# Performance work log

Hardware: AMD Instinct MI355X
Metric: run time of the kernel (lower is better)

Reference implementation:

```python
import jax, jax.numpy as jnp
import numpy as np

N = 100000
E = 1600000
NFEAT = 128
NHID = 128
NCLASS = 10


def setup_inputs() -> dict:
    key = jax.random.key(0)
    ks = jax.random.split(key, 12)
    x = jax.random.normal(ks[0], (N, NFEAT), dtype=jnp.float32)
    edge_index = jax.random.randint(ks[1], (2, E), 0, N, dtype=jnp.int64)
    s = 0.05
    W1 = jax.random.normal(ks[2], (NFEAT, NHID), dtype=jnp.float32) * s
    b1 = jnp.zeros((NHID,), dtype=jnp.float32)
    W2 = jax.random.normal(ks[3], (NHID, NHID), dtype=jnp.float32) * s
    b2 = jnp.zeros((NHID,), dtype=jnp.float32)
    W3 = jax.random.normal(ks[4], (NHID, NHID), dtype=jnp.float32) * s
    b3 = jnp.zeros((NHID,), dtype=jnp.float32)
    Wl = jax.random.normal(ks[5], (NHID, NCLASS), dtype=jnp.float32) * s
    bl = jnp.zeros((NCLASS,), dtype=jnp.float32)
    return {"x": x, "edge_index": edge_index, "W1": W1, "b1": b1,
            "W2": W2, "b2": b2, "W3": W3, "b3": b3, "Wl": Wl, "bl": bl}


def _gcn_norm(edge_index, num_nodes):
    # PyG gcn_norm with add_self_loops=True and unit edge weights.
    loops = jnp.arange(num_nodes, dtype=edge_index.dtype)
    src = jnp.concatenate([edge_index[0], loops])  # [E+N]
    dst = jnp.concatenate([edge_index[1], loops])
    ones = jnp.ones(src.shape[0], dtype=jnp.float32)
    deg = jax.ops.segment_sum(ones, dst, num_segments=num_nodes)
    dis = jax.lax.rsqrt(deg)  # deg >= 1 due to self-loops
    norm = dis[src] * dis[dst]  # [E+N]
    return src, dst, norm


def _gcn_conv(h, src, dst, norm, W, b, num_nodes):
    h = h @ W                                   # [N, out]
    msg = h[src] * norm[:, None]                # gather + edge scaling
    out = jax.ops.segment_sum(msg, dst, num_segments=num_nodes)
    return out + b


def reference(x, edge_index, W1, b1, W2, b2, W3, b3, Wl, bl):
    src, dst, norm = _gcn_norm(edge_index, N)
    h = jax.nn.relu(_gcn_conv(x, src, dst, norm, W1, b1, N))
    h = jax.nn.relu(_gcn_conv(h, src, dst, norm, W2, b2, N))
    h = _gcn_conv(h, src, dst, norm, W3, b3, N)
    logits = h @ Wl + bl                        # dropout is identity (eval / p=0)
    return jax.nn.log_softmax(logits, axis=1)
```

## Files before the change

### kernel.cpp

```cpp
#include <hip/hip_runtime.h>

#define NFEAT 128
#define NCLS  10
#define NCP   16
#define BROW  512
#define BINC  4096

static inline size_t alignup(size_t x) { return (x + 255) & ~size_t(255); }

__device__ __forceinline__ ushort f2bf(float f) {
  uint x = __float_as_uint(f);
  return (ushort)((x + 0x7fffu + ((x >> 16) & 1u)) >> 16);
}
__device__ __forceinline__ float bf2f(ushort u) {
  return __uint_as_float(((uint)u) << 16);
}

typedef short bf16x8 __attribute__((ext_vector_type(8)));
typedef float f32x4 __attribute__((ext_vector_type(4)));


__global__ void zero_ints(int* __restrict__ p, int n) {
  int i = blockIdx.x * 256 + threadIdx.x;
  if (i < n) p[i] = 0;
}

__global__ __launch_bounds__(256) void bucket_hist(const int* __restrict__ dst,
                                                   int* __restrict__ bkt_cnt,
                                                   int e, int nbkt) {
  __shared__ int hist[256];
  for (int t = threadIdx.x; t < nbkt; t += 256) hist[t] = 0;
  __syncthreads();
  int i = blockIdx.x * 256 + threadIdx.x;
  int stride = gridDim.x * 256;
  for (; i < e; i += stride) atomicAdd(&hist[dst[i] >> 9], 1);
  __syncthreads();
  for (int t = threadIdx.x; t < nbkt; t += 256)
    if (hist[t]) atomicAdd(&bkt_cnt[t], hist[t]);
}

__global__ __launch_bounds__(256) void bkt_scan(const int* __restrict__ bkt_cnt,
                                                int* __restrict__ bkt_off,
                                                int* __restrict__ gfrontier,
                                                int n, int nbkt) {
  __shared__ int sbuf[256];
  const int t = threadIdx.x;
  int x = 0;
  if (t < nbkt) {
    int lo = t << 9;
    int nodes = n - lo; if (nodes > BROW) nodes = BROW;
    x = bkt_cnt[t] + nodes;
  }
  sbuf[t] = x;
  __syncthreads();
  for (int off = 1; off < 256; off <<= 1) {
    int v = (t >= off) ? sbuf[t - off] : 0;
    __syncthreads();
    sbuf[t] += v;
    __syncthreads();
  }
  if (t < nbkt) { bkt_off[t] = sbuf[t] - x; gfrontier[t] = sbuf[t] - x; }
  if (t == nbkt - 1) bkt_off[nbkt] = sbuf[t];
}

__global__ __launch_bounds__(256) void bin_items(const int* __restrict__ ei,
                                                 int nE, int total, int nbkt,
                                                 int* __restrict__ gfrontier,
                                                 int2* __restrict__ binned) {
  __shared__ int hist[256];
  __shared__ int loff[256];
  __shared__ int gbase[256];
  __shared__ int sbuf[256];
  __shared__ int2 st[BINC];
  const int t = threadIdx.x;
  const int chunk0 = blockIdx.x * BINC;
  for (int q = t; q < nbkt; q += 256) hist[q] = 0;
  __syncthreads();
  for (int j = t; j < BINC; j += 256) {
    int i = chunk0 + j;
    if (i < total) {
      int d = (i < nE) ? ei[nE + i] : (i - nE);
      atomicAdd(&hist[d >> 9], 1);
    }
  }
  __syncthreads();
  int x = (t < nbkt) ? hist[t] : 0;
  sbuf[t] = x;
  __syncthreads();
  for (int off = 1; off < 256; off <<= 1) {
    int v = (t >= off) ? sbuf[t - off] : 0;
    __syncthreads();
    sbuf[t] += v;
    __syncthreads();
  }
  loff[t] = sbuf[t] - x;
  gbase[t] = (t < nbkt && x > 0) ? atomicAdd(&gfrontier[t], x) : 0;
  __syncthreads();
  hist[t] = loff[t];
  __syncthreads();
  for (int j = t; j < BINC; j += 256) {
    int i = chunk0 + j;
    if (i < total) {
      int s, d;
      if (i < nE) { s = ei[i]; d = ei[nE + i]; }
      else        { s = i - nE; d = s; }
      int p = atomicAdd(&hist[d >> 9], 1);
      st[p] = make_int2(s, d);
    }
  }
  __syncthreads();
  int M = total - chunk0; if (M > BINC) M = BINC;
  for (int j = t; j < M; j += 256) {
    int2 it = st[j];
    int b = it.y >> 9;
    binned[gbase[b] + (j - loff[b])] = it;
  }
}

__global__ __launch_bounds__(512) void bucket_finalize(const int2* __restrict__ binned,
                                                       const int* __restrict__ bkt_off,
                                                       int* __restrict__ row_ptr,
                                                       float* __restrict__ dis,
                                                       int* __restrict__ ev,
                                                       int n, int nbkt) {
  __shared__ int hist[BROW];
  __shared__ int sbuf[BROW];
  __shared__ int pre[BROW];
  __shared__ int front[BROW];
  const int b = blockIdx.x;
  const int t = threadIdx.x;
  const int row0 = b << 9;
  const int beg = bkt_off[b], end = bkt_off[b + 1];
  hist[t] = 0; front[t] = 0;
  __syncthreads();
  for (int j = beg + t; j < end; j += BROW)
    atomicAdd(&hist[binned[j].y - row0], 1);
  __syncthreads();
  const int x = hist[t];
  const int v = row0 + t;
  if (v < n) dis[v] = rsqrtf((float)x);
  sbuf[t] = x;
  __syncthreads();
  for (int off = 1; off < BROW; off <<= 1) {
    int val = (t >= off) ? sbuf[t - off] : 0;
    __syncthreads();
    sbuf[t] += val;
    __syncthreads();
  }
  pre[t] = sbuf[t] - x;
  if (v < n) row_ptr[v] = beg + pre[t];
  if (b == nbkt - 1 && t == 0) row_ptr[n] = end;
  __syncthreads();
  for (int j = beg + t; j < end; j += BROW) {
    int2 it = binned[j];
    int dl = it.y - row0;
    int slot = atomicAdd(&front[dl], 1);
    ev[beg + pre[dl] + slot] = it.x;
  }
}


__global__ __launch_bounds__(256) void fold_weights(const float* __restrict__ W3,
                                                    const float* __restrict__ Wl,
                                                    const float* __restrict__ b3,
                                                    const float* __restrict__ bl,
                                                    float* __restrict__ Wf,
                                                    float* __restrict__ bf) {
  int t = blockIdx.x * blockDim.x + threadIdx.x;
  if (t < NFEAT * NCP) {
    int r = t >> 4, c = t & 15;
    float s = 0.f;
    if (c < NCLS) {
      for (int k = 0; k < NFEAT; ++k) s += W3[r * NFEAT + k] * Wl[k * NCLS + c];
    }
    Wf[t] = s;
  }
  if (t < NCP) {
    float s = 0.f;
    if (t < NCLS) {
      s = bl[t];
      for (int k = 0; k < NFEAT; ++k) s += b3[k] * Wl[k * NCLS + t];
    }
    bf[t] = s;
  }
}

__global__ __launch_bounds__(256) void prep_w(const float* __restrict__ W,
                                              ushort* __restrict__ Wt) {
  int t = blockIdx.x * 256 + threadIdx.x;
  if (t < NFEAT * NFEAT) {
    int n = t >> 7, k = t & 127;
    Wt[n * NFEAT + k] = f2bf(W[k * NFEAT + n]);
  }
}


template<bool BF16IN>
__global__ __launch_bounds__(256) void gemm_mfma(const float* __restrict__ A,
                                                 const ushort* __restrict__ Ab,
                                                 const ushort* __restrict__ Wt,
                                                 const float* __restrict__ dis,
                                                 ushort* __restrict__ Cb, int nrows) {
  __shared__ __align__(16) ushort Asm[64 * NFEAT];
  const int tid = threadIdx.x;
  const int row0 = blockIdx.x * 64;
  {
    const int m = tid >> 2;
    const int kc = (tid & 3) * 32;
    const int gr = row0 + m;
    int4 u[4];
    if (BF16IN) {
      if (gr < nrows) {
        const ushort* p = Ab + (size_t)gr * NFEAT + kc;
        u[0] = *(const int4*)(p + 0);
        u[1] = *(const int4*)(p + 8);
        u[2] = *(const int4*)(p + 16);
        u[3] = *(const int4*)(p + 24);
      } else {
        u[0] = u[1] = u[2] = u[3] = make_int4(0, 0, 0, 0);
      }
    } else {
      float4 f[8];
      if (gr < nrows) {
        #pragma unroll
        for (int q = 0; q < 8; ++q)
          f[q] = *(const float4*)&A[(size_t)gr * NFEAT + kc + q * 4];
      } else {
        #pragma unroll
        for (int q = 0; q < 8; ++q) f[q] = make_float4(0.f, 0.f, 0.f, 0.f);
      }
      #pragma unroll
      for (int q = 0; q < 4; ++q) {
        union { ushort us[8]; int4 v; } pk;
        const float* fp = (const float*)&f[q * 2];
        #pragma unroll
        for (int j = 0; j < 8; ++j) pk.us[j] = f2bf(fp[j]);
        u[q] = pk.v;
      }
    }
    #pragma unroll
    for (int q = 0; q < 4; ++q) {
      int byte = (m * 256 + (kc + q * 8) * 2) ^ ((m & 7) << 4);
      *(int4*)((char*)Asm + byte) = u[q];
    }
  }
  __syncthreads();
  const int wave = tid >> 6;
  const int lane = tid & 63;
  const int m0 = wave * 16;
  bf16x8 afr[4];
  #pragma unroll
  for (int ks = 0; ks < 4; ++ks) {
    int m = m0 + (lane & 15);
    int kk = ks * 32 + (lane >> 4) * 8;
    int byte = (m * 256 + kk * 2) ^ ((m & 7) << 4);
    afr[ks] = *(const bf16x8*)((const char*)Asm + byte);
  }
  f32x4 acc[8];
  #pragma unroll
  for (int c = 0; c < 8; ++c) acc[c] = (f32x4){0.f, 0.f, 0.f, 0.f};
  #pragma unroll
  for (int c = 0; c < 8; ++c) {
    #pragma unroll
    for (int ks = 0; ks < 4; ++ks) {
      int n = c * 16 + (lane & 15);
      int kk = ks * 32 + (lane >> 4) * 8;
      bf16x8 bfr = *(const bf16x8*)&Wt[n * NFEAT + kk];
      acc[c] = __builtin_amdgcn_mfma_f32_16x16x32_bf16(afr[ks], bfr, acc[c], 0, 0, 0);
    }
  }
  const int gr_base = row0 + m0 + (lane >> 4) * 4;
  float dr[4];
  #pragma unroll
  for (int r = 0; r < 4; ++r)
    dr[r] = (gr_base + r < nrows) ? dis[gr_base + r] : 0.f;
  #pragma unroll
  for (int c = 0; c < 8; ++c) {
    #pragma unroll
    for (int r = 0; r < 4; ++r) {
      int gr = gr_base + r;
      if (gr < nrows)
        Cb[(size_t)gr * NFEAT + c * 16 + (lane & 15)] = f2bf(acc[c][r] * dr[r]);
    }
  }
}


__global__ __launch_bounds__(256) void aggregate(const ushort* __restrict__ hw,
                                                 const int* __restrict__ row_ptr,
                                                 const int* __restrict__ ev,
                                                 const float* __restrict__ dis,
                                                 const float* __restrict__ bias,
                                                 ushort* __restrict__ outb,
                                                 int relu, int n) {
  const int wave = threadIdx.x >> 6;
  const int lane = threadIdx.x & 63;
  const int v = blockIdx.x * 4 + wave;
  if (v >= n) return;
  const int beg = row_ptr[v], end = row_ptr[v + 1];
  const int half = lane >> 5;
  const int hl = lane & 31;
  float4 acc = make_float4(0.f, 0.f, 0.f, 0.f);
  int e = beg + half;
  for (; e + 6 < end; e += 8) {
    int s0 = ev[e];
    int s1 = ev[e + 2];
    int s2 = ev[e + 4];
    int s3 = ev[e + 6];
    ushort4 q0 = *(const ushort4*)&hw[(size_t)s0 * NFEAT + hl * 4];
    ushort4 q1 = *(const ushort4*)&hw[(size_t)s1 * NFEAT + hl * 4];
    ushort4 q2 = *(const ushort4*)&hw[(size_t)s2 * NFEAT + hl * 4];
    ushort4 q3 = *(const ushort4*)&hw[(size_t)s3 * NFEAT + hl * 4];
    acc.x += bf2f(q0.x) + bf2f(q1.x) + bf2f(q2.x) + bf2f(q3.x);
    acc.y += bf2f(q0.y) + bf2f(q1.y) + bf2f(q2.y) + bf2f(q3.y);
    acc.z += bf2f(q0.z) + bf2f(q1.z) + bf2f(q2.z) + bf2f(q3.z);
    acc.w += bf2f(q0.w) + bf2f(q1.w) + bf2f(q2.w) + bf2f(q3.w);
  }
  for (; e < end; e += 2) {
    int s = ev[e];
    ushort4 q = *(const ushort4*)&hw[(size_t)s * NFEAT + hl * 4];
    acc.x += bf2f(q.x); acc.y += bf2f(q.y);
    acc.z += bf2f(q.z); acc.w += bf2f(q.w);
  }
  acc.x += __shfl_xor(acc.x, 32);
  acc.y += __shfl_xor(acc.y, 32);
  acc.z += __shfl_xor(acc.z, 32);
  acc.w += __shfl_xor(acc.w, 32);
  if (half == 0) {
    float dv = dis[v];
    float4 b = *(const float4*)&bias[hl * 4];
    acc.x = fmaf(acc.x, dv, b.x); acc.y = fmaf(acc.y, dv, b.y);
    acc.z = fmaf(acc.z, dv, b.z); acc.w = fmaf(acc.w, dv, b.w);
    if (relu) {
      acc.x = fmaxf(acc.x, 0.f); acc.y = fmaxf(acc.y, 0.f);
      acc.z = fmaxf(acc.z, 0.f); acc.w = fmaxf(acc.w, 0.f);
    }
    union { ushort us[4]; uint2 q2; } pk;
    pk.us[0] = f2bf(acc.x); pk.us[1] = f2bf(acc.y);
    pk.us[2] = f2bf(acc.z); pk.us[3] = f2bf(acc.w);
    *(uint2*)&outb[(size_t)v * NFEAT + hl * 4] = pk.q2;
  }
}


__global__ __launch_bounds__(256) void gemm_small(const ushort* __restrict__ Ab,
                                                  const float* __restrict__ Wf,
                                                  const float* __restrict__ dis,
                                                  float* __restrict__ G, int n) {
  __shared__ float Ws[NFEAT * NCP];
  for (int i = threadIdx.x; i < NFEAT * NCP; i += 256) Ws[i] = Wf[i];
  __syncthreads();
  const int v = blockIdx.x * 256 + threadIdx.x;
  if (v >= n) return;
  float acc[NCP];
  #pragma unroll
  for (int c = 0; c < NCP; ++c) acc[c] = 0.f;
  #pragma unroll
  for (int p = 0; p < 8; ++p) {
    union { ushort us[16]; int4 q[2]; } a;
    const ushort* pl = Ab + (size_t)v * NFEAT + p * 16;
    a.q[0] = *(const int4*)pl;
    a.q[1] = *(const int4*)(pl + 8);
    #pragma unroll
    for (int j = 0; j < 16; ++j) {
      float av = bf2f(a.us[j]);
      int k = p * 16 + j;
      #pragma unroll
      for (int cq = 0; cq < NCP; cq += 4) {
        float4 w = *(const float4*)&Ws[k * NCP + cq];
        acc[cq + 0] += av * w.x;
        acc[cq + 1] += av * w.y;
        acc[cq + 2] += av * w.z;
        acc[cq + 3] += av * w.w;
      }
    }
  }
  const float dv = dis[v];
  #pragma unroll
  for (int cq = 0; cq < NCP; cq += 4)
    *(float4*)&G[(size_t)v * NCP + cq] =
        make_float4(acc[cq] * dv, acc[cq + 1] * dv, acc[cq + 2] * dv, acc[cq + 3] * dv);
}


__global__ __launch_bounds__(256) void agg_logits(const float* __restrict__ G,
                                                  const int* __restrict__ row_ptr,
                                                  const int* __restrict__ ev,
                                                  const float* __restrict__ dis,
                                                  const float* __restrict__ bf,
                                                  float* __restrict__ out, int n) {
  const int wave = threadIdx.x >> 6;
  const int lane = threadIdx.x & 63;
  const int v = blockIdx.x * 4 + wave;
  if (v >= n) return;
  const int beg = row_ptr[v], end = row_ptr[v + 1];
  const int g = lane >> 4;
  const int f = lane & 15;
  float acc = 0.f;
  int e = beg + g;
  for (; e + 4 < end; e += 8) {
    int s0 = ev[e];
    int s1 = ev[e + 4];
    acc += G[(size_t)s0 * NCP + f] + G[(size_t)s1 * NCP + f];
  }
  for (; e < end; e += 4) {
    acc += G[(size_t)ev[e] * NCP + f];
  }
  acc += __shfl_xor(acc, 16);
  acc += __shfl_xor(acc, 32);
  float logit = dis[v] * acc + bf[f];
  float pv = (f < NCLS) ? logit : -INFINITY;
  float m = pv;
  #pragma unroll
  for (int s = 8; s >= 1; s >>= 1) m = fmaxf(m, __shfl_xor(m, s));
  float ex = (f < NCLS) ? expf(logit - m) : 0.f;
  float ssum = ex;
  #pragma unroll
  for (int s = 8; s >= 1; s >>= 1) ssum += __shfl_xor(ssum, s);
  float lse = m + logf(ssum);
  if (g == 0 && f < NCLS) out[(size_t)v * NCLS + f] = logit - lse;
}


extern "C" void kernel_launch(void* const* d_in, const int* in_sizes, int n_in,
                              void* d_out, int out_size, void* d_ws, size_t ws_size,
                              hipStream_t stream) {
  const float* x  = (const float*)d_in[0];
  const int*   ei = (const int*)d_in[1];
  const float* W1 = (const float*)d_in[2];
  const float* b1 = (const float*)d_in[3];
  const float* W2 = (const float*)d_in[4];
  const float* b2 = (const float*)d_in[5];
  const float* W3 = (const float*)d_in[6];
  const float* b3 = (const float*)d_in[7];
  const float* Wl = (const float*)d_in[8];
  const float* bl = (const float*)d_in[9];
  float* out = (float*)d_out;

  const int nN = in_sizes[0] / NFEAT;
  const int nE = in_sizes[1] / 2;
  const int total = nN + nE;
  const int nbkt = (nN + BROW - 1) >> 9;
  const int nbBin = (total + BINC - 1) / BINC;

  char* ws = (char*)d_ws;
  int*    bkt_cnt = (int*)ws;     ws += alignup(256 * 4);
  int*    bkt_off = (int*)ws;     ws += alignup(257 * 4);
  int*    gfront  = (int*)ws;     ws += alignup(256 * 4);
  int*    row_ptr = (int*)ws;     ws += alignup((size_t)(nN + 1) * 4);
  float*  dis     = (float*)ws;   ws += alignup((size_t)nN * 4);
  float*  Wf      = (float*)ws;   ws += alignup((size_t)NFEAT * NCP * 4);
  float*  bfv     = (float*)ws;   ws += alignup((size_t)NCP * 4);
  ushort* Wt1     = (ushort*)ws;  ws += alignup((size_t)NFEAT * NFEAT * 2);
  ushort* Wt2     = (ushort*)ws;  ws += alignup((size_t)NFEAT * NFEAT * 2);
  int2*   binned  = (int2*)ws;    ws += alignup((size_t)total * 8);
  int*    ev      = (int*)ws;     ws += alignup((size_t)total * 4);
  ushort* hb      = (ushort*)ws;  ws += alignup((size_t)nN * NFEAT * 2);
  ushort* hbA     = (ushort*)ws;  ws += alignup((size_t)nN * NFEAT * 2);
  float*  G       = (float*)ws;   ws += alignup((size_t)nN * NCP * 4);

  zero_ints<<<1, 256, 0, stream>>>(bkt_cnt, nbkt);
  bucket_hist<<<512, 256, 0, stream>>>(ei + nE, bkt_cnt, nE, nbkt);
  bkt_scan<<<1, 256, 0, stream>>>(bkt_cnt, bkt_off, gfront, nN, nbkt);
  bin_items<<<nbBin, 256, 0, stream>>>(ei, nE, total, nbkt, gfront, binned);
  bucket_finalize<<<nbkt, BROW, 0, stream>>>(binned, bkt_off, row_ptr, dis, ev, nN, nbkt);

  fold_weights<<<8, 256, 0, stream>>>(W3, Wl, b3, bl, Wf, bfv);
  prep_w<<<64, 256, 0, stream>>>(W1, Wt1);
  prep_w<<<64, 256, 0, stream>>>(W2, Wt2);

  const int gemm_grid = (nN + 63) / 64;
  const int node_grid = (nN + 3) / 4;

  gemm_mfma<false><<<gemm_grid, 256, 0, stream>>>(x, nullptr, Wt1, dis, hb, nN);
  aggregate<<<node_grid, 256, 0, stream>>>(hb, row_ptr, ev, dis, b1, hbA, 1, nN);
  gemm_mfma<true><<<gemm_grid, 256, 0, stream>>>(nullptr, hbA, Wt2, dis, hb, nN);
  aggregate<<<node_grid, 256, 0, stream>>>(hb, row_ptr, ev, dis, b2, hbA, 1, nN);
  gemm_small<<<(nN + 255) / 256, 256, 0, stream>>>(hbA, Wf, dis, G, nN);
  agg_logits<<<node_grid, 256, 0, stream>>>(G, row_ptr, ev, dis, bfv, out, nN);
}
```

Measured before the change: 355.6 us.

## Split hidden features into two column planes for aggregation; store logit messages in bf16

```diff
diff --git a/kernel.cpp b/kernel.cpp
--- a/kernel.cpp
+++ b/kernel.cpp
@@ -19,11 +19,6 @@
 typedef short bf16x8 __attribute__((ext_vector_type(8)));
 typedef float f32x4 __attribute__((ext_vector_type(4)));
 
-
-__global__ void zero_ints(int* __restrict__ p, int n) {
-  int i = blockIdx.x * 256 + threadIdx.x;
-  if (i < n) p[i] = 0;
-}
 
 __global__ __launch_bounds__(256) void bucket_hist(const int* __restrict__ dst,
                                                    int* __restrict__ bkt_cnt,
@@ -185,13 +180,15 @@
   }
 }
 
-__global__ __launch_bounds__(256) void prep_w(const float* __restrict__ W,
-                                              ushort* __restrict__ Wt) {
+__global__ __launch_bounds__(256) void prep_w2(const float* __restrict__ W1,
+                                               const float* __restrict__ W2,
+                                               ushort* __restrict__ Wt1,
+                                               ushort* __restrict__ Wt2) {
   int t = blockIdx.x * 256 + threadIdx.x;
-  if (t < NFEAT * NFEAT) {
-    int n = t >> 7, k = t & 127;
-    Wt[n * NFEAT + k] = f2bf(W[k * NFEAT + n]);
-  }
+  int u = t & 16383;
+  int n = u >> 7, k = u & 127;
+  if (t < 16384) Wt1[n * NFEAT + k] = f2bf(W1[k * NFEAT + n]);
+  else           Wt2[n * NFEAT + k] = f2bf(W2[k * NFEAT + n]);
 }
 
 
@@ -200,7 +197,8 @@
                                                  const ushort* __restrict__ Ab,
                                                  const ushort* __restrict__ Wt,
                                                  const float* __restrict__ dis,
-                                                 ushort* __restrict__ Cb, int nrows) {
+                                                 ushort* __restrict__ outS,
+                                                 size_t pstride, int nrows) {
   __shared__ __align__(16) ushort Asm[64 * NFEAT];
   const int tid = threadIdx.x;
   const int row0 = blockIdx.x * 64;
@@ -276,59 +274,59 @@
     dr[r] = (gr_base + r < nrows) ? dis[gr_base + r] : 0.f;
   #pragma unroll
   for (int c = 0; c < 8; ++c) {
+    ushort* plane = outS + (size_t)(c >> 2) * pstride;
+    const int fcol = (c & 3) * 16 + (lane & 15);
     #pragma unroll
     for (int r = 0; r < 4; ++r) {
       int gr = gr_base + r;
       if (gr < nrows)
-        Cb[(size_t)gr * NFEAT + c * 16 + (lane & 15)] = f2bf(acc[c][r] * dr[r]);
-    }
-  }
-}
-
-
-__global__ __launch_bounds__(256) void aggregate(const ushort* __restrict__ hw,
+        plane[(size_t)gr * 64 + fcol] = f2bf(acc[c][r] * dr[r]);
+    }
+  }
+}
+
+
+__global__ __launch_bounds__(256) void aggregate(const ushort* __restrict__ hbS,
                                                  const int* __restrict__ row_ptr,
                                                  const int* __restrict__ ev,
                                                  const float* __restrict__ dis,
                                                  const float* __restrict__ bias,
                                                  ushort* __restrict__ outb,
-                                                 int relu, int n) {
+                                                 size_t pstride, int relu, int n) {
+  const int slice = blockIdx.x & 1;
   const int wave = threadIdx.x >> 6;
   const int lane = threadIdx.x & 63;
-  const int v = blockIdx.x * 4 + wave;
+  const int v = (blockIdx.x >> 1) * 4 + wave;
   if (v >= n) return;
   const int beg = row_ptr[v], end = row_ptr[v + 1];
-  const int half = lane >> 5;
-  const int hl = lane & 31;
+  const int qg = lane >> 4;
+  const int hl = lane & 15;
+  const ushort* plane = hbS + (size_t)slice * pstride;
   float4 acc = make_float4(0.f, 0.f, 0.f, 0.f);
-  int e = beg + half;
-  for (; e + 6 < end; e += 8) {
+  int e = beg + qg;
+  for (; e + 4 < end; e += 8) {
     int s0 = ev[e];
-    int s1 = ev[e + 2];
-    int s2 = ev[e + 4];
-    int s3 = ev[e + 6];
-    ushort4 q0 = *(const ushort4*)&hw[(size_t)s0 * NFEAT + hl * 4];
-    ushort4 q1 = *(const ushort4*)&hw[(size_t)s1 * NFEAT + hl * 4];
-    ushort4 q2 = *(const ushort4*)&hw[(size_t)s2 * NFEAT + hl * 4];
-    ushort4 q3 = *(const ushort4*)&hw[(size_t)s3 * NFEAT + hl * 4];
-    acc.x += bf2f(q0.x) + bf2f(q1.x) + bf2f(q2.x) + bf2f(q3.x);
-    acc.y += bf2f(q0.y) + bf2f(q1.y) + bf2f(q2.y) + bf2f(q3.y);
-    acc.z += bf2f(q0.z) + bf2f(q1.z) + bf2f(q2.z) + bf2f(q3.z);
-    acc.w += bf2f(q0.w) + bf2f(q1.w) + bf2f(q2.w) + bf2f(q3.w);
-  }
-  for (; e < end; e += 2) {
+    int s1 = ev[e + 4];
+    ushort4 q0 = *(const ushort4*)&plane[(size_t)s0 * 64 + hl * 4];
+    ushort4 q1 = *(const ushort4*)&plane[(size_t)s1 * 64 + hl * 4];
+    acc.x += bf2f(q0.x) + bf2f(q1.x);
+    acc.y += bf2f(q0.y) + bf2f(q1.y);
+    acc.z += bf2f(q0.z) + bf2f(q1.z);
+    acc.w += bf2f(q0.w) + bf2f(q1.w);
+  }
+  for (; e < end; e += 4) {
     int s = ev[e];
-    ushort4 q = *(const ushort4*)&hw[(size_t)s * NFEAT + hl * 4];
+    ushort4 q = *(const ushort4*)&plane[(size_t)s * 64 + hl * 4];
     acc.x += bf2f(q.x); acc.y += bf2f(q.y);
     acc.z += bf2f(q.z); acc.w += bf2f(q.w);
   }
-  acc.x += __shfl_xor(acc.x, 32);
-  acc.y += __shfl_xor(acc.y, 32);
-  acc.z += __shfl_xor(acc.z, 32);
-  acc.w += __shfl_xor(acc.w, 32);
-  if (half == 0) {
+  acc.x += __shfl_xor(acc.x, 16); acc.x += __shfl_xor(acc.x, 32);
+  acc.y += __shfl_xor(acc.y, 16); acc.y += __shfl_xor(acc.y, 32);
+  acc.z += __shfl_xor(acc.z, 16); acc.z += __shfl_xor(acc.z, 32);
+  acc.w += __shfl_xor(acc.w, 16); acc.w += __shfl_xor(acc.w, 32);
+  if (qg == 0) {
     float dv = dis[v];
-    float4 b = *(const float4*)&bias[hl * 4];
+    float4 b = *(const float4*)&bias[slice * 64 + hl * 4];
     acc.x = fmaf(acc.x, dv, b.x); acc.y = fmaf(acc.y, dv, b.y);
     acc.z = fmaf(acc.z, dv, b.z); acc.w = fmaf(acc.w, dv, b.w);
     if (relu) {
@@ -338,7 +336,7 @@
     union { ushort us[4]; uint2 q2; } pk;
     pk.us[0] = f2bf(acc.x); pk.us[1] = f2bf(acc.y);
     pk.us[2] = f2bf(acc.z); pk.us[3] = f2bf(acc.w);
-    *(uint2*)&outb[(size_t)v * NFEAT + hl * 4] = pk.q2;
+    *(uint2*)&outb[(size_t)v * NFEAT + slice * 64 + hl * 4] = pk.q2;
   }
 }
 
@@ -346,7 +344,7 @@
 __global__ __launch_bounds__(256) void gemm_small(const ushort* __restrict__ Ab,
                                                   const float* __restrict__ Wf,
                                                   const float* __restrict__ dis,
-                                                  float* __restrict__ G, int n) {
+                                                  ushort* __restrict__ Gb, int n) {
   __shared__ float Ws[NFEAT * NCP];
   for (int i = threadIdx.x; i < NFEAT * NCP; i += 256) Ws[i] = Wf[i];
   __syncthreads();
@@ -376,14 +374,15 @@
     }
   }
   const float dv = dis[v];
-  #pragma unroll
-  for (int cq = 0; cq < NCP; cq += 4)
-    *(float4*)&G[(size_t)v * NCP + cq] =
-        make_float4(acc[cq] * dv, acc[cq + 1] * dv, acc[cq + 2] * dv, acc[cq + 3] * dv);
-}
-
-
-__global__ __launch_bounds__(256) void agg_logits(const float* __restrict__ G,
+  union { ushort us[16]; int4 q[2]; } pk;
+  #pragma unroll
+  for (int c = 0; c < NCP; ++c) pk.us[c] = f2bf(acc[c] * dv);
+  *(int4*)&Gb[(size_t)v * NCP + 0] = pk.q[0];
+  *(int4*)&Gb[(size_t)v * NCP + 8] = pk.q[1];
+}
+
+
+__global__ __launch_bounds__(256) void agg_logits(const ushort* __restrict__ Gb,
                                                   const int* __restrict__ row_ptr,
                                                   const int* __restrict__ ev,
                                                   const float* __restrict__ dis,
@@ -401,10 +400,10 @@
   for (; e + 4 < end; e += 8) {
     int s0 = ev[e];
     int s1 = ev[e + 4];
-    acc += G[(size_t)s0 * NCP + f] + G[(size_t)s1 * NCP + f];
+    acc += bf2f(Gb[(size_t)s0 * NCP + f]) + bf2f(Gb[(size_t)s1 * NCP + f]);
   }
   for (; e < end; e += 4) {
-    acc += G[(size_t)ev[e] * NCP + f];
+    acc += bf2f(Gb[(size_t)ev[e] * NCP + f]);
   }
   acc += __shfl_xor(acc, 16);
   acc += __shfl_xor(acc, 32);
@@ -442,6 +441,7 @@
   const int total = nN + nE;
   const int nbkt = (nN + BROW - 1) >> 9;
   const int nbBin = (total + BINC - 1) / BINC;
+  const size_t pstride = (size_t)nN * 64;
 
   char* ws = (char*)d_ws;
   int*    bkt_cnt = (int*)ws;     ws += alignup(256 * 4);
@@ -455,27 +455,27 @@
   ushort* Wt2     = (ushort*)ws;  ws += alignup((size_t)NFEAT * NFEAT * 2);
   int2*   binned  = (int2*)ws;    ws += alignup((size_t)total * 8);
   int*    ev      = (int*)ws;     ws += alignup((size_t)total * 4);
-  ushort* hb      = (ushort*)ws;  ws += alignup((size_t)nN * NFEAT * 2);
+  ushort* hbS     = (ushort*)ws;  ws += alignup((size_t)nN * NFEAT * 2);
   ushort* hbA     = (ushort*)ws;  ws += alignup((size_t)nN * NFEAT * 2);
-  float*  G       = (float*)ws;   ws += alignup((size_t)nN * NCP * 4);
-
-  zero_ints<<<1, 256, 0, stream>>>(bkt_cnt, nbkt);
+  ushort* Gb      = (ushort*)ws;  ws += alignup((size_t)nN * NCP * 2);
+
+  hipMemsetAsync(bkt_cnt, 0, 256 * sizeof(int), stream);
   bucket_hist<<<512, 256, 0, stream>>>(ei + nE, bkt_cnt, nE, nbkt);
   bkt_scan<<<1, 256, 0, stream>>>(bkt_cnt, bkt_off, gfront, nN, nbkt);
   bin_items<<<nbBin, 256, 0, stream>>>(ei, nE, total, nbkt, gfront, binned);
   bucket_finalize<<<nbkt, BROW, 0, stream>>>(binned, bkt_off, row_ptr, dis, ev, nN, nbkt);
 
   fold_weights<<<8, 256, 0, stream>>>(W3, Wl, b3, bl, Wf, bfv);
-  prep_w<<<64, 256, 0, stream>>>(W1, Wt1);
-  prep_w<<<64, 256, 0, stream>>>(W2, Wt2);
+  prep_w2<<<128, 256, 0, stream>>>(W1, W2, Wt1, Wt2);
 
   const int gemm_grid = (nN + 63) / 64;
   const int node_grid = (nN + 3) / 4;
-
-  gemm_mfma<false><<<gemm_grid, 256, 0, stream>>>(x, nullptr, Wt1, dis, hb, nN);
-  aggregate<<<node_grid, 256, 0, stream>>>(hb, row_ptr, ev, dis, b1, hbA, 1, nN);
-  gemm_mfma<true><<<gemm_grid, 256, 0, stream>>>(nullptr, hbA, Wt2, dis, hb, nN);
-  aggregate<<<node_grid, 256, 0, stream>>>(hb, row_ptr, ev, dis, b2, hbA, 1, nN);
-  gemm_small<<<(nN + 255) / 256, 256, 0, stream>>>(hbA, Wf, dis, G, nN);
-  agg_logits<<<node_grid, 256, 0, stream>>>(G, row_ptr, ev, dis, bfv, out, nN);
-}
+  const int agg_grid = node_grid * 2;
+
+  gemm_mfma<false><<<gemm_grid, 256, 0, stream>>>(x, nullptr, Wt1, dis, hbS, pstride, nN);
+  aggregate<<<agg_grid, 256, 0, stream>>>(hbS, row_ptr, ev, dis, b1, hbA, pstride, 1, nN);
+  gemm_mfma<true><<<gemm_grid, 256, 0, stream>>>(nullptr, hbA, Wt2, dis, hbS, pstride, nN);
+  aggregate<<<agg_grid, 256, 0, stream>>>(hbS, row_ptr, ev, dis, b2, hbA, pstride, 1, nN);
+  gemm_small<<<(nN + 255) / 256, 256, 0, stream>>>(hbA, Wf, dis, Gb, nN);
+  agg_logits<<<node_grid, 256, 0, stream>>>(Gb, row_ptr, ev, dis, bfv, out, nN);
+}
```

Result: slower. 407.8 us (+14.7%).
